# Optimization experiments

Hardware: AMD Instinct MI355X
Metric: run time of the kernel (lower is better)

## Reference

```python
import jax, jax.numpy as jnp
import numpy as np

B, N, D, H = 8, 1024, 1024, 16
DH = D // H
EPS = 1e-6


def setup_inputs() -> dict:
    key = jax.random.key(0)
    ks = jax.random.split(key, 12)
    s = 1.0 / np.sqrt(D)
    inp = {
        "x": jax.random.normal(ks[0], (B, N, D), jnp.float32),
        "y": jax.random.normal(ks[1], (B, N, D), jnp.float32),
        "Wq": jax.random.normal(ks[2], (D, D), jnp.float32) * s,
        "bq": jnp.zeros((D,), jnp.float32),
        "Wk": jax.random.normal(ks[3], (D, D), jnp.float32) * s,
        "bk": jnp.zeros((D,), jnp.float32),
        "Wv": jax.random.normal(ks[4], (D, D), jnp.float32) * s,
        "bv": jnp.zeros((D,), jnp.float32),
        "Wf": jax.random.normal(ks[5], (D, D), jnp.float32) * s,
        "bf": jnp.zeros((D,), jnp.float32),
        "g1": jnp.ones((D,), jnp.float32),
        "b1": jnp.zeros((D,), jnp.float32),
        "g2": jnp.ones((D,), jnp.float32),
        "b2": jnp.zeros((D,), jnp.float32),
    }
    return inp


def _layernorm(x, g, b):
    mu = jnp.mean(x, axis=-1, keepdims=True)
    var = jnp.mean(jnp.square(x - mu), axis=-1, keepdims=True)
    return (x - mu) * jax.lax.rsqrt(var + EPS) * g + b


def reference(x, y, Wq, bq, Wk, bk, Wv, bv, Wf, bf, g1, b1, g2, b2):
    q = x @ Wq + bq                      # [B, Nq, D]
    k = y @ Wk + bk                      # [B, Nk, D]
    v = y @ Wv + bv                      # [B, Nk, D]
    qh = q.reshape(B, N, H, DH)
    kh = k.reshape(B, N, H, DH)
    vh = v.reshape(B, N, H, DH)
    # NOTE: original scales by sqrt(embed_dim), not sqrt(head_dim)
    scores = jnp.einsum("bqhd,bkhd->bhqk", qh, kh) / jnp.sqrt(jnp.float32(D))
    att = jax.nn.softmax(scores, axis=-1)
    o = jnp.einsum("bhqk,bkhd->bqhd", att, vh).reshape(B, N, D)
    out = x + o
    out = _layernorm(out, g1, b1)
    out = out + jax.nn.relu(out @ Wf + bf)
    out = _layernorm(out, g2, b2)
    return out
```

## Files before the change

### kernel.cpp

```cpp
#include <hip/hip_runtime.h>


#define Bb 8
#define Nn 1024
#define Dd 1024
#define Hh 16
#define DH 64
#define Mrows (Bb * 1024)

#define QSCL 0.045084220027780106f

typedef float f32x4 __attribute__((ext_vector_type(4)));
typedef __bf16 bf16x8 __attribute__((ext_vector_type(8)));
typedef unsigned int u32x4 __attribute__((ext_vector_type(4)));

#define MFMA16(acc, a, b) \
  acc = __builtin_amdgcn_mfma_f32_16x16x32_bf16((a), (b), (acc), 0, 0, 0)

__device__ __forceinline__ bf16x8 ld_frag(const void* p) {
  u32x4 v = *(const u32x4*)p;
  return __builtin_bit_cast(bf16x8, v);
}

__device__ __forceinline__ void gload16(const void* g, void* l) {
  __builtin_amdgcn_global_load_lds(
      (const __attribute__((address_space(1))) unsigned int*)g,
      (__attribute__((address_space(3))) unsigned int*)l, 16, 0, 0);
}

__device__ __forceinline__ unsigned short f2bf(float f) {
  return __builtin_bit_cast(unsigned short, (__bf16)f);
}
__device__ __forceinline__ float bf2f(unsigned short s) {
  unsigned int u = ((unsigned int)s) << 16;
  return __builtin_bit_cast(float, u);
}
__device__ __forceinline__ unsigned cvt_pk_bf16(float a, float b) {
  unsigned r;
  asm("v_cvt_pk_bf16_f32 %0, %1, %2" : "=v"(r) : "v"(a), "v"(b));
  return r;
}

__global__ __launch_bounds__(256) void prep(
    const float* __restrict__ x, const float* __restrict__ y,
    unsigned short* __restrict__ xb, unsigned short* __restrict__ yb,
    const float* __restrict__ W0, const float* __restrict__ W1,
    const float* __restrict__ W2, const float* __restrict__ W3,
    unsigned short* __restrict__ T0, unsigned short* __restrict__ T1,
    unsigned short* __restrict__ T2, unsigned short* __restrict__ T3) {
  __shared__ float tile[32][33];
  const int z = blockIdx.z, t = threadIdx.x;
  if (z < 2) {
    const float* in = z ? y : x;
    unsigned short* out = z ? yb : xb;
    const int n4 = (Mrows * Dd) / 4;
    int i = blockIdx.x * 256 + t;
    int stride = 1024 * 256;
    for (; i < n4; i += stride) {
      float4 v = ((const float4*)in)[i];
      ushort4 o;
      o.x = f2bf(v.x); o.y = f2bf(v.y); o.z = f2bf(v.z); o.w = f2bf(v.w);
      ((ushort4*)out)[i] = o;
    }
  } else {
    const float* W = z == 2 ? W0 : z == 3 ? W1 : z == 4 ? W2 : W3;
    unsigned short* Wt = z == 2 ? T0 : z == 3 ? T1 : z == 4 ? T2 : T3;
    const int tx = t & 31, ty = t >> 5;
    const int n0 = (blockIdx.x & 31) * 32, k0 = (blockIdx.x >> 5) * 32;
#pragma unroll
    for (int i = ty; i < 32; i += 8)
      tile[i][tx] = W[(size_t)(k0 + i) * Dd + n0 + tx];
    __syncthreads();
#pragma unroll
    for (int i = ty; i < 32; i += 8)
      Wt[(size_t)(n0 + i) * Dd + k0 + tx] = f2bf(tile[tx][i]);
  }
}

struct GemmCtx { int m0, n0, wm, wn, lr, lk, lg, l, w; };

template <typename EpiFn>
__device__ __forceinline__ void gemm_core(
    const unsigned short* __restrict__ A, const unsigned short* __restrict__ Bt,
    int K, EpiFn epi) {
  __shared__ __attribute__((aligned(16))) unsigned short As[2][128 * 32];
  __shared__ __attribute__((aligned(16))) unsigned short Bs[2][128 * 32];
  const int bid = blockIdx.y * 8 + blockIdx.x;
  const int nwg = (gridDim.x * gridDim.y);
  const int swz = (bid & 7) * (nwg >> 3) + (bid >> 3);
  const int m0 = (swz >> 3) * 128, n0 = (swz & 7) * 128;
  const int t = threadIdx.x, w = t >> 6, l = t & 63;
  const int wm = (w >> 1) * 64, wn = (w & 1) * 64;
  const int lr = l & 15, lk = (l >> 4) * 8;
  const int rA = t >> 2, sA = (t & 3) * 8;
  char* AsB = (char*)As;
  char* BsB = (char*)Bs;
  const int wb = (w * 64) * 16;

  f32x4 acc[4][4] = {};

  for (int k0 = 0; k0 < K; k0 += 64) {
    __syncthreads();
#pragma unroll
    for (int h = 0; h < 2; ++h) {
      const int ko = k0 + h * 32;
      gload16(A + (size_t)(m0 + rA) * K + ko + sA, AsB + h * 8192 + wb);
      gload16(A + (size_t)(m0 + 64 + rA) * K + ko + sA, AsB + h * 8192 + wb + 4096);
      gload16(Bt + (size_t)(n0 + rA) * K + ko + sA, BsB + h * 8192 + wb);
      gload16(Bt + (size_t)(n0 + 64 + rA) * K + ko + sA, BsB + h * 8192 + wb + 4096);
    }
    __syncthreads();

#pragma unroll
    for (int h = 0; h < 2; ++h) {
      bf16x8 af[4], bfr[4];
#pragma unroll
      for (int i = 0; i < 4; ++i)
        af[i] = ld_frag(&As[h][(wm + i * 16 + lr) * 32 + lk]);
#pragma unroll
      for (int j = 0; j < 4; ++j)
        bfr[j] = ld_frag(&Bs[h][(wn + j * 16 + lr) * 32 + lk]);
#pragma unroll
      for (int i = 0; i < 4; ++i)
#pragma unroll
        for (int j = 0; j < 4; ++j) MFMA16(acc[i][j], af[i], bfr[j]);
    }
  }
  GemmCtx c{m0, n0, wm, wn, lr, lk, l >> 4, l, w};
  epi(acc, c);
}

__global__ __launch_bounds__(256) void gemm_qkv(
    const unsigned short* __restrict__ xb, const unsigned short* __restrict__ yb,
    const unsigned short* __restrict__ WqT, const unsigned short* __restrict__ WkT,
    const unsigned short* __restrict__ WvT,
    const float* __restrict__ bq, const float* __restrict__ bk,
    const float* __restrict__ bv,
    unsigned short* __restrict__ Qb, unsigned short* __restrict__ Kb,
    unsigned short* __restrict__ Vtb) {
  const int z = blockIdx.z;
  const unsigned short* A = (z == 0) ? xb : yb;
  const unsigned short* Bt = (z == 0) ? WqT : (z == 1) ? WkT : WvT;
  const float* bias = (z == 0) ? bq : (z == 1) ? bk : bv;
  unsigned short* Cb = (z == 0) ? Qb : Kb;

  gemm_core(A, Bt, Dd, [&](f32x4 (&acc)[4][4], GemmCtx c) {
#pragma unroll
    for (int i = 0; i < 4; ++i)
#pragma unroll
      for (int j = 0; j < 4; ++j) {
        int col = c.n0 + c.wn + j * 16 + c.lr;
        float bcol = bias[col];
        if (z == 2) {
          int brow = c.m0 + c.wm + i * 16 + c.lg * 4;
          int bi = brow >> 10, nloc = brow & 1023;
          int nperm = (nloc & ~31) | (((nloc >> 2) & 3) << 3) |
                      (((nloc >> 4) & 1) << 2);
          ushort4 o4;
          o4.x = f2bf(acc[i][j][0] + bcol);
          o4.y = f2bf(acc[i][j][1] + bcol);
          o4.z = f2bf(acc[i][j][2] + bcol);
          o4.w = f2bf(acc[i][j][3] + bcol);
          *(ushort4*)(Vtb + ((size_t)bi * Dd + col) * Nn + nperm) = o4;
        } else {
          float scl = (z == 0) ? QSCL : 1.0f;
#pragma unroll
          for (int r = 0; r < 4; ++r) {
            int row = c.m0 + c.wm + i * 16 + c.lg * 4 + r;
            Cb[(size_t)row * Dd + col] = f2bf((acc[i][j][r] + bcol) * scl);
          }
        }
      }
  });
}

__global__ __launch_bounds__(256) void gemm_ff(
    const unsigned short* __restrict__ A, const unsigned short* __restrict__ Bt,
    const float* __restrict__ bias, const unsigned short* __restrict__ Tres,
    unsigned short* __restrict__ Cb) {
  gemm_core(A, Bt, Dd, [&](f32x4 (&acc)[4][4], GemmCtx c) {
#pragma unroll
    for (int i = 0; i < 4; ++i)
#pragma unroll
      for (int j = 0; j < 4; ++j) {
        int col = c.n0 + c.wn + j * 16 + c.lr;
        float bcol = bias[col];
#pragma unroll
        for (int r = 0; r < 4; ++r) {
          int row = c.m0 + c.wm + i * 16 + c.lg * 4 + r;
          size_t idx = (size_t)row * Dd + col;
          Cb[idx] = f2bf(bf2f(Tres[idx]) + fmaxf(acc[i][j][r] + bcol, 0.f));
        }
      }
  });
}

__global__ __launch_bounds__(512) void attn_fwd(
    const unsigned short* __restrict__ Qg, const unsigned short* __restrict__ Kg,
    const unsigned short* __restrict__ Vt, unsigned short* __restrict__ Obf) {
  __shared__ __attribute__((aligned(16))) unsigned short KVs[2][2][64 * 64];
  char* lbase = (char*)KVs;

  const int bid = blockIdx.y * 4 + blockIdx.x;
  const int swz = (bid & 7) * 64 + (bid >> 3);
  const int q0 = (swz & 3) * 256;
  const int by = swz >> 2;
  const int b = by >> 4, h = by & 15;

  const int t = threadIdx.x, w = t >> 6, l = t & 63;
  const int lr = l & 15, lg = l >> 4;

  bf16x8 aq[2][2];
#pragma unroll
  for (int i = 0; i < 2; ++i) {
    const unsigned short* qp =
        Qg + ((size_t)b * Nn + q0 + w * 32 + i * 16 + lr) * Dd + h * DH + lg * 8;
    aq[i][0] = *(const bf16x8*)qp;
    aq[i][1] = *(const bf16x8*)(qp + 32);
  }

  u32x4 one4 = {0x3F803F80u, 0x3F803F80u, 0x3F803F80u, 0x3F803F80u};
  const bf16x8 vones = __builtin_bit_cast(bf16x8, one4);

  const size_t baseK = (size_t)b * Nn * Dd + h * DH;
  const size_t baseV = ((size_t)b * Dd + h * DH) * Nn;

  const int srow = t >> 3, sch = t & 7;
  const int sby = srow * 128 + ((sch * 16) ^ ((srow & 7) << 4));

  uint4 kA = *(const uint4*)(Kg + baseK + (size_t)srow * Dd + sch * 8);
  uint4 vA = *(const uint4*)(Vt + baseV + (size_t)srow * Nn + sch * 8);

  *(uint4*)(lbase + sby) = kA;
  *(uint4*)(lbase + 8192 + sby) = vA;
  __syncthreads();

  f32x4 oacc[4][2] = {};
  f32x4 lacc[2] = {};

  for (int kv = 0; kv < Nn / 64; ++kv) {
    char* kcur = lbase + (kv & 1) * 16384;
    char* vcur = kcur + 8192;
    const bool more = (kv + 1) < Nn / 64;
    if (more) {
      int kvo = (kv + 1) * 64;
      kA = *(const uint4*)(Kg + baseK + (size_t)(kvo + srow) * Dd + sch * 8);
      vA = *(const uint4*)(Vt + baseV + (size_t)srow * Nn + kvo + sch * 8);
    }

    f32x4 st[2][4];
    __builtin_amdgcn_s_setprio(1);
#pragma unroll
    for (int j = 0; j < 4; ++j) {
      const int kro = (j * 16 + lr) * 128;
      bf16x8 k0 = ld_frag(kcur + kro + (((lg ^ (lr & 7))) << 4));
      bf16x8 k1 = ld_frag(kcur + kro + ((((lg + 4) ^ (lr & 7))) << 4));
#pragma unroll
      for (int i = 0; i < 2; ++i) {
        f32x4 z = {0.f, 0.f, 0.f, 0.f};
        MFMA16(z, k0, aq[i][0]);
        MFMA16(z, k1, aq[i][1]);
        st[i][j] = z;
      }
    }
    __builtin_amdgcn_s_setprio(0);

#pragma unroll
    for (int i = 0; i < 2; ++i)
#pragma unroll
      for (int j = 0; j < 4; ++j) {
        st[i][j][0] = exp2f(st[i][j][0]);
        st[i][j][1] = exp2f(st[i][j][1]);
        st[i][j][2] = exp2f(st[i][j][2]);
        st[i][j][3] = exp2f(st[i][j][3]);
      }

#pragma unroll
    for (int m = 0; m < 2; ++m) {
      bf16x8 pb[2];
#pragma unroll
      for (int i = 0; i < 2; ++i) {
        u32x4 pk;
        pk[0] = cvt_pk_bf16(st[i][2 * m][0], st[i][2 * m][1]);
        pk[1] = cvt_pk_bf16(st[i][2 * m][2], st[i][2 * m][3]);
        pk[2] = cvt_pk_bf16(st[i][2 * m + 1][0], st[i][2 * m + 1][1]);
        pk[3] = cvt_pk_bf16(st[i][2 * m + 1][2], st[i][2 * m + 1][3]);
        pb[i] = __builtin_bit_cast(bf16x8, pk);
      }
      __builtin_amdgcn_s_setprio(1);
      MFMA16(lacc[0], vones, pb[0]);
      MFMA16(lacc[1], vones, pb[1]);
#pragma unroll
      for (int da = 0; da < 4; ++da) {
        const int vrow = da * 16 + lr;
        bf16x8 va = ld_frag(
            vcur + vrow * 128 + (((lg + 4 * m) ^ (vrow & 7)) << 4));
        MFMA16(oacc[da][0], va, pb[0]);
        MFMA16(oacc[da][1], va, pb[1]);
      }
      __builtin_amdgcn_s_setprio(0);
    }

    if (more) {
      char* knxt = lbase + ((kv + 1) & 1) * 16384;
      *(uint4*)(knxt + sby) = kA;
      *(uint4*)(knxt + 8192 + sby) = vA;
      __syncthreads();
    }
  }

#pragma unroll
  for (int i = 0; i < 2; ++i) {
    float rd = 1.f / lacc[i][0];
    const size_t orow = (size_t)b * Nn + q0 + w * 32 + i * 16 + lr;
#pragma unroll
    for (int da = 0; da < 4; ++da) {
      ushort4 o4;
      o4.x = f2bf(oacc[da][i][0] * rd);
      o4.y = f2bf(oacc[da][i][1] * rd);
      o4.z = f2bf(oacc[da][i][2] * rd);
      o4.w = f2bf(oacc[da][i][3] * rd);
      *(ushort4*)(Obf + orow * Dd + h * DH + da * 16 + lg * 4) = o4;
    }
  }
}

template <int MODE>
__global__ __launch_bounds__(256) void ln_k(
    const unsigned short* __restrict__ X, const unsigned short* __restrict__ Oin,
    const float* __restrict__ gamma, const float* __restrict__ beta,
    unsigned short* __restrict__ out_bf, float* __restrict__ out_f) {
  __shared__ float red[8];
  const int row = blockIdx.x, t = threadIdx.x;
  ushort4 xu = ((const ushort4*)(X + (size_t)row * Dd))[t];
  float4 v = {bf2f(xu.x), bf2f(xu.y), bf2f(xu.z), bf2f(xu.w)};
  if (MODE == 0) {
    ushort4 o = ((const ushort4*)(Oin + (size_t)row * Dd))[t];
    v.x += bf2f(o.x); v.y += bf2f(o.y); v.z += bf2f(o.z); v.w += bf2f(o.w);
  }
  float s = v.x + v.y + v.z + v.w;
#pragma unroll
  for (int o = 32; o > 0; o >>= 1) s += __shfl_xor(s, o, 64);
  if ((t & 63) == 0) red[t >> 6] = s;
  __syncthreads();
  float mean = (red[0] + red[1] + red[2] + red[3]) * (1.f / 1024.f);
  float dx = v.x - mean, dy = v.y - mean, dz = v.z - mean, dw = v.w - mean;
  float s2 = dx * dx + dy * dy + dz * dz + dw * dw;
#pragma unroll
  for (int o = 32; o > 0; o >>= 1) s2 += __shfl_xor(s2, o, 64);
  if ((t & 63) == 0) red[4 + (t >> 6)] = s2;
  __syncthreads();
  float var = (red[4] + red[5] + red[6] + red[7]) * (1.f / 1024.f);
  float rstd = rsqrtf(var + 1e-6f);
  float4 g = ((const float4*)gamma)[t];
  float4 bb = ((const float4*)beta)[t];
  float r0 = dx * rstd * g.x + bb.x;
  float r1 = dy * rstd * g.y + bb.y;
  float r2 = dz * rstd * g.z + bb.z;
  float r3 = dw * rstd * g.w + bb.w;
  if (MODE == 0) {
    ushort4 o4;
    o4.x = f2bf(r0); o4.y = f2bf(r1); o4.z = f2bf(r2); o4.w = f2bf(r3);
    ((ushort4*)(out_bf + (size_t)row * Dd))[t] = o4;
  } else {
    float4 o4 = {r0, r1, r2, r3};
    ((float4*)(out_f + (size_t)row * Dd))[t] = o4;
  }
}

extern "C" void kernel_launch(void* const* d_in, const int* in_sizes, int n_in,
                              void* d_out, int out_size, void* d_ws, size_t ws_size,
                              hipStream_t stream) {
  const float* x  = (const float*)d_in[0];
  const float* y  = (const float*)d_in[1];
  const float* Wq = (const float*)d_in[2];
  const float* bq = (const float*)d_in[3];
  const float* Wk = (const float*)d_in[4];
  const float* bk = (const float*)d_in[5];
  const float* Wv = (const float*)d_in[6];
  const float* bv = (const float*)d_in[7];
  const float* Wf = (const float*)d_in[8];
  const float* bf = (const float*)d_in[9];
  const float* g1 = (const float*)d_in[10];
  const float* b1 = (const float*)d_in[11];
  const float* g2 = (const float*)d_in[12];
  const float* b2 = (const float*)d_in[13];

  char* ws = (char*)d_ws;
  const size_t MB = 1024 * 1024;
  unsigned short* xb  = (unsigned short*)(ws + 0 * MB);
  unsigned short* yb  = (unsigned short*)(ws + 16 * MB);
  unsigned short* WqT = (unsigned short*)(ws + 32 * MB);
  unsigned short* WkT = (unsigned short*)(ws + 34 * MB);
  unsigned short* WvT = (unsigned short*)(ws + 36 * MB);
  unsigned short* WfT = (unsigned short*)(ws + 38 * MB);
  unsigned short* Qb  = (unsigned short*)(ws + 40 * MB);
  unsigned short* Kb  = (unsigned short*)(ws + 56 * MB);
  unsigned short* Vtb = (unsigned short*)(ws + 72 * MB);
  unsigned short* Obf = (unsigned short*)(ws + 16 * MB);
  unsigned short* tb  = (unsigned short*)(ws + 40 * MB);
  unsigned short* ub  = (unsigned short*)(ws + 56 * MB);

  prep<<<dim3(1024, 1, 6), 256, 0, stream>>>(
      x, y, xb, yb, Wq, Wk, Wv, Wf, WqT, WkT, WvT, WfT);

  gemm_qkv<<<dim3(8, 64, 3), 256, 0, stream>>>(
      xb, yb, WqT, WkT, WvT, bq, bk, bv, Qb, Kb, Vtb);

  attn_fwd<<<dim3(4, 128), 512, 0, stream>>>(Qb, Kb, Vtb, Obf);

  ln_k<0><<<Mrows, 256, 0, stream>>>(xb, Obf, g1, b1, tb, nullptr);

  gemm_ff<<<dim3(8, 64), 256, 0, stream>>>(tb, WfT, bf, tb, ub);

  ln_k<1><<<Mrows, 256, 0, stream>>>(ub, nullptr, g2, b2, nullptr, (float*)d_out);
}
```

Before: 195.9 us.

## Double-buffer LDS tiles in GEMM core to overlap loads with MFMA

The shared GEMM mainloop now keeps two LDS buffers for the A and B tiles. It issues the global-to-LDS loads for tile k+1 before computing on tile k, and needs only one barrier per iteration instead of two. The aim is to hide global-load latency behind the matrix-core work in the QKV and FFN projections. In exchange, LDS per block doubles to 64 KB, which can lower occupancy. A local variable in the attention kernel is also renamed, with no effect on speed.

```diff
diff --git a/kernel.cpp b/kernel.cpp
--- a/kernel.cpp
+++ b/kernel.cpp
@@ -83,8 +83,8 @@
 __device__ __forceinline__ void gemm_core(
     const unsigned short* __restrict__ A, const unsigned short* __restrict__ Bt,
     int K, EpiFn epi) {
-  __shared__ __attribute__((aligned(16))) unsigned short As[2][128 * 32];
-  __shared__ __attribute__((aligned(16))) unsigned short Bs[2][128 * 32];
+  __shared__ __attribute__((aligned(16))) unsigned short As[2][2][128 * 32];
+  __shared__ __attribute__((aligned(16))) unsigned short Bs[2][2][128 * 32];
   const int bid = blockIdx.y * 8 + blockIdx.x;
   const int nwg = (gridDim.x * gridDim.y);
   const int swz = (bid & 7) * (nwg >> 3) + (bid >> 3);
@@ -93,38 +93,46 @@
   const int wm = (w >> 1) * 64, wn = (w & 1) * 64;
   const int lr = l & 15, lk = (l >> 4) * 8;
   const int rA = t >> 2, sA = (t & 3) * 8;
-  char* AsB = (char*)As;
-  char* BsB = (char*)Bs;
   const int wb = (w * 64) * 16;
 
-  f32x4 acc[4][4] = {};
-
-  for (int k0 = 0; k0 < K; k0 += 64) {
-    __syncthreads();
+  auto stage = [&](int d, int k0) {
 #pragma unroll
     for (int h = 0; h < 2; ++h) {
       const int ko = k0 + h * 32;
-      gload16(A + (size_t)(m0 + rA) * K + ko + sA, AsB + h * 8192 + wb);
-      gload16(A + (size_t)(m0 + 64 + rA) * K + ko + sA, AsB + h * 8192 + wb + 4096);
-      gload16(Bt + (size_t)(n0 + rA) * K + ko + sA, BsB + h * 8192 + wb);
-      gload16(Bt + (size_t)(n0 + 64 + rA) * K + ko + sA, BsB + h * 8192 + wb + 4096);
-    }
-    __syncthreads();
-
+      char* ab = (char*)&As[d][h][0];
+      char* bb = (char*)&Bs[d][h][0];
+      gload16(A + (size_t)(m0 + rA) * K + ko + sA, ab + wb);
+      gload16(A + (size_t)(m0 + 64 + rA) * K + ko + sA, ab + wb + 4096);
+      gload16(Bt + (size_t)(n0 + rA) * K + ko + sA, bb + wb);
+      gload16(Bt + (size_t)(n0 + 64 + rA) * K + ko + sA, bb + wb + 4096);
+    }
+  };
+
+  f32x4 acc[4][4] = {};
+
+  stage(0, 0);
+  __syncthreads();
+
+  const int nt = K >> 6;
+#pragma unroll 1
+  for (int tt = 0; tt < nt; ++tt) {
+    if (tt + 1 < nt) stage((tt + 1) & 1, (tt + 1) * 64);
+    const int d = tt & 1;
 #pragma unroll
     for (int h = 0; h < 2; ++h) {
       bf16x8 af[4], bfr[4];
 #pragma unroll
       for (int i = 0; i < 4; ++i)
-        af[i] = ld_frag(&As[h][(wm + i * 16 + lr) * 32 + lk]);
+        af[i] = ld_frag(&As[d][h][(wm + i * 16 + lr) * 32 + lk]);
 #pragma unroll
       for (int j = 0; j < 4; ++j)
-        bfr[j] = ld_frag(&Bs[h][(wn + j * 16 + lr) * 32 + lk]);
+        bfr[j] = ld_frag(&Bs[d][h][(wn + j * 16 + lr) * 32 + lk]);
 #pragma unroll
       for (int i = 0; i < 4; ++i)
 #pragma unroll
         for (int j = 0; j < 4; ++j) MFMA16(acc[i][j], af[i], bfr[j]);
     }
+    __syncthreads();
   }
   GemmCtx c{m0, n0, wm, wn, lr, lk, l >> 4, l, w};
   epi(acc, c);
@@ -257,10 +265,10 @@
       bf16x8 k1 = ld_frag(kcur + kro + ((((lg + 4) ^ (lr & 7))) << 4));
 #pragma unroll
       for (int i = 0; i < 2; ++i) {
-        f32x4 z = {0.f, 0.f, 0.f, 0.f};
-        MFMA16(z, k0, aq[i][0]);
-        MFMA16(z, k1, aq[i][1]);
-        st[i][j] = z;
+        f32x4 zz = {0.f, 0.f, 0.f, 0.f};
+        MFMA16(zz, k0, aq[i][0]);
+        MFMA16(zz, k1, aq[i][1]);
+        st[i][j] = zz;
       }
     }
     __builtin_amdgcn_s_setprio(0);
```

Result: no change. 198.3 us (+1.2%).
